# Optimization experiments

Hardware: AMD Instinct MI355X
Metric: run time of the kernel (lower is better)

Reference implementation:

```python
import jax, jax.numpy as jnp
import numpy as np

MIN_DEPTH, MAX_DEPTH = 0.1, 100.0
BN_EPS = 1e-5


def _conv(x, w, b, pad):
    y = jax.lax.conv_general_dilated(
        x, w, window_strides=(1, 1), padding=[(pad, pad), (pad, pad)],
        dimension_numbers=("NCHW", "OIHW", "NCHW"))
    return y + b[None, :, None, None]


def _bn(x, gamma, beta, mean, var):
    # eval-mode BatchNorm2d with running stats
    inv = jax.lax.rsqrt(var + BN_EPS)
    return (x - mean[None, :, None, None]) * (gamma * inv)[None, :, None, None] + beta[None, :, None, None]


def _object_depths(depth, bboxes):
    # depth: (B,1,H,W), bboxes: (B,N,4) int — per-box median (lower median, like torch)
    B, _, H, W = depth.shape
    xs = jnp.arange(W)
    ys = jnp.arange(H)

    def per_image(d2, boxes):  # d2: (H,W), boxes: (N,4)
        dflat = d2.reshape(-1)

        def one_box(box):
            x1 = jnp.maximum(box[0], 0)
            y1 = jnp.maximum(box[1], 0)
            x2 = jnp.minimum(box[2], W)
            y2 = jnp.minimum(box[3], H)
            mask = (((ys >= y1) & (ys < y2))[:, None] & ((xs >= x1) & (xs < x2))[None, :]).reshape(-1)
            vals = jnp.where(mask, dflat, jnp.inf)
            s = jnp.sort(vals)
            k = mask.sum()
            idx = jnp.maximum((k - 1) // 2, 0)
            med = jnp.take(s, idx)
            return jnp.where(k > 0, med, jnp.zeros((), dtype=d2.dtype))

        return jax.vmap(one_box)(boxes)

    return jax.vmap(per_image)(depth[:, 0], bboxes)


def _forward(features, bboxes, w1, b1, g1, be1, m1, v1, w2, b2, g2, be2, m2, v2,
             w3, b3, uw1, ub1, uw2, ub2):
    # depth head
    h = jax.nn.relu(_bn(_conv(features, w1, b1, 1), g1, be1, m1, v1))
    h = jax.nn.relu(_bn(_conv(h, w2, b2, 1), g2, be2, m2, v2))
    disp = jax.nn.sigmoid(_conv(h, w3, b3, 0))  # (B,1,H,W)
    min_disp = 1.0 / MAX_DEPTH
    max_disp = 1.0 / MIN_DEPTH
    depth = 1.0 / (min_disp + (max_disp - min_disp) * disp)
    # uncertainty head
    u = jax.nn.relu(_conv(features, uw1, ub1, 1))
    uncertainty = jax.nn.softplus(_conv(u, uw2, ub2, 0))
    obj = _object_depths(depth, bboxes)
    return depth, uncertainty, obj


def setup_inputs() -> dict:
    key = jax.random.key(0)
    ks = jax.random.split(key, 16)
    B, C, Hc, H, W, N = 8, 256, 256, 96, 160, 64
    f32 = jnp.float32
    inp = {
        "features": jax.random.normal(ks[0], (B, C, H, W), dtype=f32),
        "bboxes": jax.random.randint(ks[1], (B, N, 4), 0, 96, dtype=jnp.int32),
        "w1": jax.random.normal(ks[2], (Hc, C, 3, 3), dtype=f32) * 0.02,
        "b1": jnp.zeros((Hc,), f32),
        "g1": jnp.ones((Hc,), f32),
        "be1": jnp.zeros((Hc,), f32),
        "m1": jax.random.normal(ks[3], (Hc,), dtype=f32) * 0.1,
        "v1": jnp.ones((Hc,), f32),
        "w2": jax.random.normal(ks[4], (Hc, Hc, 3, 3), dtype=f32) * 0.02,
        "b2": jnp.zeros((Hc,), f32),
        "g2": jnp.ones((Hc,), f32),
        "be2": jnp.zeros((Hc,), f32),
        "m2": jax.random.normal(ks[5], (Hc,), dtype=f32) * 0.1,
        "v2": jnp.ones((Hc,), f32),
        "w3": jax.random.normal(ks[6], (1, Hc, 1, 1), dtype=f32) * 0.05,
        "b3": jnp.zeros((1,), f32),
        "uw1": jax.random.normal(ks[7], (Hc // 2, C, 3, 3), dtype=f32) * 0.02,
        "ub1": jnp.zeros((Hc // 2,), f32),
        "uw2": jax.random.normal(ks[8], (1, Hc // 2, 1, 1), dtype=f32) * 0.05,
        "ub2": jnp.zeros((1,), f32),
    }
    return inp


def reference(features, bboxes, w1, b1, g1, be1, m1, v1, w2, b2, g2, be2, m2, v2,
              w3, b3, uw1, ub1, uw2, ub2):
    return _forward(features, bboxes, w1, b1, g1, be1, m1, v1, w2, b2, g2, be2,
                    m2, v2, w3, b3, uw1, ub1, uw2, ub2)
```

## Files before the change

### kernel.cpp

```cpp
#include <hip/hip_runtime.h>
#include <hip/hip_bf16.h>

#define HH 96
#define WW 160
#define BATCH 8
#define NPIX (BATCH*HH*WW)
#define CIN 256
#define IMG (HH*WW)
#define PW 162
#define PH 98
#define PR (PH*PW)
#define PTOT (BATCH*PR)

typedef short bf16x8 __attribute__((ext_vector_type(8)));
typedef float f32x4 __attribute__((ext_vector_type(4)));

__device__ __forceinline__ unsigned short f2bf(float f) {
    unsigned int u = __float_as_uint(f);
    u = (u + 0x7fffu + ((u >> 16) & 1u)) >> 16;
    return (unsigned short)u;
}

__device__ __forceinline__ void gload16(const void* g, void* l) {
    __builtin_amdgcn_global_load_lds(
        (const __attribute__((address_space(1))) void*)g,
        (__attribute__((address_space(3))) void*)l,
        16, 0, 0);
}

__global__ __launch_bounds__(256) void prep_scalars(
    const float* __restrict__ b1, const float* __restrict__ g1, const float* __restrict__ be1,
    const float* __restrict__ m1, const float* __restrict__ v1,
    const float* __restrict__ b2, const float* __restrict__ g2, const float* __restrict__ be2,
    const float* __restrict__ m2, const float* __restrict__ v2,
    const float* __restrict__ ub1,
    float* __restrict__ scale1, float* __restrict__ bias1,
    float* __restrict__ scale2, float* __restrict__ bias2)
{
    int t = threadIdx.x;
    float s1 = g1[t] * rsqrtf(v1[t] + 1e-5f);
    scale1[t] = s1;
    bias1[t]  = (b1[t] - m1[t]) * s1 + be1[t];
    float s2 = g2[t] * rsqrtf(v2[t] + 1e-5f);
    scale2[t] = s2;
    bias2[t]  = (b2[t] - m2[t]) * s2 + be2[t];
    if (t < 128) { scale1[256 + t] = 1.0f; bias1[256 + t] = ub1[t]; }
}

__global__ __launch_bounds__(256) void prep_weights(
    const float* __restrict__ w1, const float* __restrict__ w2, const float* __restrict__ uw1,
    unsigned short* __restrict__ w1T, unsigned short* __restrict__ w2T, unsigned short* __restrict__ uw1T)
{
    const int S = 256 * 2304;
    int i = blockIdx.x * 256 + threadIdx.x;
    if (i < S) {
        int co = i / 2304, r = i % 2304, pos = r >> 8, ci = r & 255;
        w1T[i] = f2bf(w1[(co * 256 + ci) * 9 + pos]);
    } else if (i < 2 * S) {
        int j = i - S;
        int co = j / 2304, r = j % 2304, pos = r >> 8, ci = r & 255;
        w2T[j] = f2bf(w2[(co * 256 + ci) * 9 + pos]);
    } else {
        int j = i - 2 * S;
        int co = j / 2304, r = j % 2304, pos = r >> 8, ci = r & 255;
        uw1T[j] = f2bf(uw1[(co * 256 + ci) * 9 + pos]);
    }
}

__global__ __launch_bounds__(128) void zero_pads(
    unsigned int* __restrict__ featP, unsigned int* __restrict__ h1P)
{
    int bid = blockIdx.x;
    unsigned int* buf = (bid < 4128) ? featP : h1P;
    int k = (bid < 4128) ? bid : (bid - 4128);
    int img = k / 516, i = k % 516;
    int py, px;
    if (i < PW)            { py = 0;      px = i; }
    else if (i < 2 * PW)   { py = PH - 1; px = i - PW; }
    else { int q = i - 2 * PW; py = 1 + (q >> 1); px = (q & 1) ? (PW - 1) : 0; }
    size_t row = (size_t)img * PR + (size_t)py * PW + px;
    buf[row * 128 + threadIdx.x] = 0;
}

__global__ __launch_bounds__(256) void pack_features(
    const float* __restrict__ f, unsigned short* __restrict__ ft)
{
    __shared__ float tile[32][33];
    int x0 = blockIdx.x * 32;
    int c0 = blockIdx.y * 32;
    int by = blockIdx.z;
    int b = by / HH, y = by % HH;
    int tx = threadIdx.x & 31, tg = threadIdx.x >> 5;
    const float* src = f + (((size_t)(b * CIN + c0) * HH + y) * WW) + x0;
    #pragma unroll
    for (int i = 0; i < 4; ++i) {
        int cl = tg + i * 8;
        tile[cl][tx] = src[(size_t)cl * HH * WW + tx];
    }
    __syncthreads();
    size_t rbase = (size_t)b * PR + (size_t)(y + 1) * PW + (x0 + 1);
    #pragma unroll
    for (int i = 0; i < 4; ++i) {
        int xl = tg + i * 8;
        ft[(rbase + xl) * 256 + c0 + tx] = f2bf(tile[tx][xl]);
    }
}

__global__ __launch_bounds__(256, 3) void conv3x3_mfma(
    const unsigned short* __restrict__ inP,
    const unsigned short* __restrict__ wT,
    const float* __restrict__ scale, const float* __restrict__ bias,
    unsigned short* __restrict__ outT,
    float* __restrict__ uout,
    const float* __restrict__ uw2, const float* __restrict__ ub2,
    int Cout, int mode, int My)
{
    __shared__ unsigned short Alds[3 * 128 * 32];
    __shared__ unsigned short Blds[144 * 32];
    __shared__ float usum[2][128];

    const int t = threadIdx.x;
    const int wave = t >> 6;
    const int l = t & 63;

    const int lid = blockIdx.x;
    const int xcd = lid & 7;
    const int j = lid >> 3;
    const int n0 = (xcd * 120 + j / My) * 128;
    const int m0 = (j % My) * 128;
    const bool is_unc = (mode == 1) && (m0 == 256);

    const int b0 = n0 / IMG;
    const int rem0 = n0 % IMG;
    const int y0 = rem0 / WW;
    const int x0 = rem0 % WW;
    const int r0 = b0 * PR + (y0 + 1) * PW + (x0 + 1);

    const int lrow = l >> 2;
    const int lkq = (l & 3) ^ ((l >> 3) & 3);

    const unsigned short* asrc0 = wT + (size_t)(m0 + wave * 32 + lrow) * 9 * 256 + lkq * 8;
    const unsigned short* asrc1 = asrc0 + (size_t)16 * 9 * 256;

    char* AldsB = (char*)Alds;
    char* BldsB = (char*)Blds;
    char* aldst = AldsB + wave * 2048;

    const int wm = wave >> 1, wn = wave & 1;
    const int quad = l >> 4, lane16 = l & 15;
    const int aoff = lane16 * 64 + ((quad ^ ((lane16 >> 1) & 3)) << 4);

    int browbase[4];
    #pragma unroll
    for (int i = 0; i < 4; ++i) {
        int jj = wn * 64 + i * 16 + lane16;
        browbase[i] = jj + ((x0 + jj) >= WW ? 2 : 0) + 7;
    }

    f32x4 acc[4][4];
    #pragma unroll
    for (int mt = 0; mt < 4; ++mt)
        #pragma unroll
        for (int nt = 0; nt < 4; ++nt)
            acc[mt][nt] = (f32x4){0.f, 0.f, 0.f, 0.f};

    for (int cc = 0; cc < 8; ++cc) {
        const int ccoff = cc * 32;
        for (int dyi = 0; dyi < 3; ++dyi) {
            __syncthreads();
            const unsigned short* a0 = asrc0 + (dyi * 3) * 256 + ccoff;
            const unsigned short* a1 = asrc1 + (dyi * 3) * 256 + ccoff;
            #pragma unroll
            for (int dxp = 0; dxp < 3; ++dxp) {
                gload16(a0 + dxp * 256, aldst + dxp * 8192);
                gload16(a1 + dxp * 256, aldst + dxp * 8192 + 1024);
            }
            const ptrdiff_t rs = (ptrdiff_t)r0 + (ptrdiff_t)(dyi - 1) * PW - 8;
            const unsigned short* bs = inP + (rs + lrow) * 256 + ccoff + lkq * 8
                                           + (size_t)wave * 8192;
            gload16(bs, BldsB + wave * 2048);
            gload16(bs + 4096, BldsB + wave * 2048 + 1024);
            if (wave == 3) gload16(bs + 8192, BldsB + 8192);
            __syncthreads();
            #pragma unroll
            for (int dx = 0; dx < 3; ++dx) {
                bf16x8 af[4], bfr[4];
                #pragma unroll
                for (int mt = 0; mt < 4; ++mt)
                    af[mt] = *(const bf16x8*)(AldsB + dx * 8192 + ((wm * 4 + mt) << 10) + aoff);
                #pragma unroll
                for (int i = 0; i < 4; ++i) {
                    int row = browbase[i] + dx;
                    int ba = (row << 6) + ((quad ^ ((row >> 1) & 3)) << 4);
                    bfr[i] = *(const bf16x8*)(BldsB + ba);
                }
                #pragma unroll
                for (int mt = 0; mt < 4; ++mt)
                    #pragma unroll
                    for (int nt = 0; nt < 4; ++nt)
                        acc[mt][nt] = __builtin_amdgcn_mfma_f32_16x16x32_bf16(
                            af[mt], bfr[nt], acc[mt][nt], 0, 0, 0);
            }
        }
    }

    if (is_unc) {
        const float* ub = bias + 256;
        float s[4] = {0.f, 0.f, 0.f, 0.f};
        #pragma unroll
        for (int mt = 0; mt < 4; ++mt) {
            const int mg = wm * 64 + mt * 16 + quad * 4;
            const float4 bi = *(const float4*)&ub[mg];
            const float4 uw = *(const float4*)&uw2[mg];
            #pragma unroll
            for (int nt = 0; nt < 4; ++nt) {
                s[nt] += fmaxf(acc[mt][nt][0] + bi.x, 0.f) * uw.x
                       + fmaxf(acc[mt][nt][1] + bi.y, 0.f) * uw.y
                       + fmaxf(acc[mt][nt][2] + bi.z, 0.f) * uw.z
                       + fmaxf(acc[mt][nt][3] + bi.w, 0.f) * uw.w;
            }
        }
        #pragma unroll
        for (int nt = 0; nt < 4; ++nt) {
            s[nt] += __shfl_xor(s[nt], 16);
            s[nt] += __shfl_xor(s[nt], 32);
        }
        if (quad == 0) {
            #pragma unroll
            for (int nt = 0; nt < 4; ++nt)
                usum[wm][wn * 64 + nt * 16 + lane16] = s[nt];
        }
        __syncthreads();
        if (t < 128) {
            float x = usum[0][t] + usum[1][t] + ub2[0];
            uout[n0 + t] = fmaxf(x, 0.f) + log1pf(expf(-fabsf(x)));
        }
        return;
    }

    size_t obase[4];
    #pragma unroll
    for (int nt = 0; nt < 4; ++nt) {
        int n = n0 + wn * 64 + nt * 16 + lane16;
        if (mode == 1) {
            int b = n / IMG, rem = n % IMG, yy = rem / WW, xx = rem % WW;
            obase[nt] = ((size_t)(b * PH + yy + 1) * PW + (xx + 1)) * 256;
        } else {
            obase[nt] = (size_t)n * Cout;
        }
    }
    #pragma unroll
    for (int mt = 0; mt < 4; ++mt) {
        const int mg = m0 + wm * 64 + mt * 16 + quad * 4;
        const float4 sc = *(const float4*)&scale[mg];
        const float4 bi = *(const float4*)&bias[mg];
        #pragma unroll
        for (int nt = 0; nt < 4; ++nt) {
            ushort4 pk;
            pk.x = f2bf(fmaxf(acc[mt][nt][0] * sc.x + bi.x, 0.f));
            pk.y = f2bf(fmaxf(acc[mt][nt][1] * sc.y + bi.y, 0.f));
            pk.z = f2bf(fmaxf(acc[mt][nt][2] * sc.z + bi.z, 0.f));
            pk.w = f2bf(fmaxf(acc[mt][nt][3] * sc.w + bi.w, 0.f));
            *(ushort4*)&outT[obase[nt] + mg] = pk;
        }
    }
}

__global__ __launch_bounds__(256) void head_depth(
    const unsigned short* __restrict__ h2, const float* __restrict__ w3,
    const float* __restrict__ b3, float* __restrict__ out)
{
    __shared__ float ws[256];
    ws[threadIdx.x] = w3[threadIdx.x];
    __syncthreads();
    const int pix = blockIdx.x * 64 + (threadIdx.x >> 2);
    const int q = threadIdx.x & 3;
    const unsigned short* p = h2 + (size_t)pix * 256 + q * 64;
    float s = 0.f;
    #pragma unroll
    for (int i = 0; i < 64; i += 8) {
        uint4 v = *(const uint4*)(p + i);
        const float* wq = &ws[q * 64 + i];
        s += __uint_as_float(v.x << 16) * wq[0];
        s += __uint_as_float(v.x & 0xffff0000u) * wq[1];
        s += __uint_as_float(v.y << 16) * wq[2];
        s += __uint_as_float(v.y & 0xffff0000u) * wq[3];
        s += __uint_as_float(v.z << 16) * wq[4];
        s += __uint_as_float(v.z & 0xffff0000u) * wq[5];
        s += __uint_as_float(v.w << 16) * wq[6];
        s += __uint_as_float(v.w & 0xffff0000u) * wq[7];
    }
    s += __shfl_xor(s, 1);
    s += __shfl_xor(s, 2);
    if (q == 0) {
        float x = s + b3[0];
        float sig = 1.f / (1.f + expf(-x));
        out[pix] = 1.f / (0.01f + 9.99f * sig);
    }
}

__global__ __launch_bounds__(256) void median_kernel(
    const float* __restrict__ depth, const int* __restrict__ bboxes, float* __restrict__ obj)
{
    const int bi = blockIdx.x;
    const int b = bi >> 6;
    const int* bb = bboxes + (size_t)bi * 4;
    int x1 = max(bb[0], 0), y1 = max(bb[1], 0);
    int x2 = min(bb[2], WW), y2 = min(bb[3], HH);
    int w = x2 - x1, h = y2 - y1;
    if (w <= 0 || h <= 0) {
        if (threadIdx.x == 0) obj[bi] = 0.f;
        return;
    }
    const int wh = w * h;
    int tgt = (wh - 1) >> 1;
    const float* dbase = depth + (size_t)b * HH * WW;

    __shared__ unsigned int hist[256];
    __shared__ unsigned int sel_prefix, sel_target;
    unsigned int prefix = 0;

    for (int pass = 0; pass < 4; ++pass) {
        const int shift = 24 - 8 * pass;
        hist[threadIdx.x] = 0;
        __syncthreads();
        const unsigned int mask_high = (pass == 0) ? 0u : (0xFFFFFFFFu << (shift + 8));
        for (int idx = threadIdx.x; idx < wh; idx += 256) {
            int yy = y1 + idx / w, xx = x1 + idx % w;
            unsigned int uu = __float_as_uint(dbase[yy * WW + xx]);
            if ((uu & mask_high) == (prefix & mask_high))
                atomicAdd(&hist[(uu >> shift) & 255], 1u);
        }
        __syncthreads();
        if (threadIdx.x == 0) {
            unsigned int cum = 0;
            for (int bin = 0; bin < 256; ++bin) {
                unsigned int c = hist[bin];
                if (cum + c > (unsigned int)tgt) {
                    sel_target = (unsigned int)tgt - cum;
                    sel_prefix = prefix | ((unsigned int)bin << shift);
                    break;
                }
                cum += c;
            }
        }
        __syncthreads();
        prefix = sel_prefix;
        tgt = (int)sel_target;
    }
    if (threadIdx.x == 0) obj[bi] = __uint_as_float(prefix);
}

extern "C" void kernel_launch(void* const* d_in, const int* in_sizes, int n_in,
                              void* d_out, int out_size, void* d_ws, size_t ws_size,
                              hipStream_t stream) {
    const float* features = (const float*)d_in[0];
    const int*   bboxes   = (const int*)d_in[1];
    const float* w1  = (const float*)d_in[2];
    const float* b1  = (const float*)d_in[3];
    const float* g1  = (const float*)d_in[4];
    const float* be1 = (const float*)d_in[5];
    const float* m1  = (const float*)d_in[6];
    const float* v1  = (const float*)d_in[7];
    const float* w2  = (const float*)d_in[8];
    const float* b2  = (const float*)d_in[9];
    const float* g2  = (const float*)d_in[10];
    const float* be2 = (const float*)d_in[11];
    const float* m2  = (const float*)d_in[12];
    const float* v2  = (const float*)d_in[13];
    const float* w3  = (const float*)d_in[14];
    const float* b3  = (const float*)d_in[15];
    const float* uw1 = (const float*)d_in[16];
    const float* ub1 = (const float*)d_in[17];
    const float* uw2 = (const float*)d_in[18];
    const float* ub2 = (const float*)d_in[19];
    float* out = (float*)d_out;

    char* ws = (char*)d_ws;
    unsigned short* featP = (unsigned short*)(ws + 8192);
    unsigned short* h1P   = (unsigned short*)(ws + 65044480);
    unsigned short* h2    = (unsigned short*)(ws + 8192);
    unsigned short* w1T   = (unsigned short*)(ws + 130080768);
    unsigned short* uw1T  = w1T + 256 * 2304;
    unsigned short* w2T   = uw1T + 128 * 2304;
    float* scale1 = (float*)(w2T + 589824);
    float* bias1  = scale1 + 384;
    float* scale2 = bias1 + 384;
    float* bias2  = scale2 + 256;

    prep_scalars<<<1, 256, 0, stream>>>(b1, g1, be1, m1, v1, b2, g2, be2, m2, v2, ub1,
                                        scale1, bias1, scale2, bias2);
    prep_weights<<<5760, 256, 0, stream>>>(w1, w2, uw1, w1T, w2T, uw1T);
    zero_pads<<<8256, 128, 0, stream>>>((unsigned int*)featP, (unsigned int*)h1P);
    pack_features<<<dim3(WW / 32, CIN / 32, BATCH * HH), 256, 0, stream>>>(features, featP);

    conv3x3_mfma<<<2880, 256, 0, stream>>>(
        featP, w1T, scale1, bias1, h1P, out + NPIX, uw2, ub2, 256, 1, 3);
    conv3x3_mfma<<<1920, 256, 0, stream>>>(
        h1P, w2T, scale2, bias2, h2, nullptr, nullptr, nullptr, 256, 0, 2);

    head_depth<<<NPIX / 64, 256, 0, stream>>>(h2, w3, b3, out);
    median_kernel<<<BATCH * 64, 256, 0, stream>>>(out, bboxes, out + 2 * NPIX);
}
```

Measured before the change: 649.7 us.

## Fuse depth 1x1 projection into conv2 epilogue with atomic reduction

The second conv now computes the 1x1 depth projection directly in its epilogue: each block reduces BN+ReLU outputs against w3 and atomically adds its partial dot product into a zero-initialized depth buffer, so the bf16 h2 tensor is never written or reread. A small elementwise kernel then applies the bias, sigmoid and depth mapping. The zero_pads kernel additionally clears the depth output. The first conv also gets a higher min-waves launch bound (4 instead of 3), which may force register spilling. Atomics make the summation order nondeterministic.

Measured after the change: 629.1 us. 1.03x faster.

```diff
diff --git a/kernel.cpp b/kernel.cpp
--- a/kernel.cpp
+++ b/kernel.cpp
@@ -68,18 +68,23 @@
 }
 
 __global__ __launch_bounds__(128) void zero_pads(
-    unsigned int* __restrict__ featP, unsigned int* __restrict__ h1P)
+    unsigned int* __restrict__ featP, unsigned int* __restrict__ h1P, float* __restrict__ outd)
 {
     int bid = blockIdx.x;
-    unsigned int* buf = (bid < 4128) ? featP : h1P;
-    int k = (bid < 4128) ? bid : (bid - 4128);
-    int img = k / 516, i = k % 516;
-    int py, px;
-    if (i < PW)            { py = 0;      px = i; }
-    else if (i < 2 * PW)   { py = PH - 1; px = i - PW; }
-    else { int q = i - 2 * PW; py = 1 + (q >> 1); px = (q & 1) ? (PW - 1) : 0; }
-    size_t row = (size_t)img * PR + (size_t)py * PW + px;
-    buf[row * 128 + threadIdx.x] = 0;
+    if (bid < 8256) {
+        unsigned int* buf = (bid < 4128) ? featP : h1P;
+        int k = (bid < 4128) ? bid : (bid - 4128);
+        int img = k / 516, i = k % 516;
+        int py, px;
+        if (i < PW)            { py = 0;      px = i; }
+        else if (i < 2 * PW)   { py = PH - 1; px = i - PW; }
+        else { int q = i - 2 * PW; py = 1 + (q >> 1); px = (q & 1) ? (PW - 1) : 0; }
+        size_t row = (size_t)img * PR + (size_t)py * PW + px;
+        buf[row * 128 + threadIdx.x] = 0;
+    } else {
+        int k = bid - 8256;
+        outd[(size_t)k * 128 + threadIdx.x] = 0.f;
+    }
 }
 
 __global__ __launch_bounds__(256) void pack_features(
@@ -106,7 +111,8 @@
     }
 }
 
-__global__ __launch_bounds__(256, 3) void conv3x3_mfma(
+template<int MINW>
+__global__ __launch_bounds__(256, MINW) void conv3x3_mfma(
     const unsigned short* __restrict__ inP,
     const unsigned short* __restrict__ wT,
     const float* __restrict__ scale, const float* __restrict__ bias,
@@ -238,16 +244,43 @@
         return;
     }
 
+    if (mode == 0) {
+        float s[4] = {0.f, 0.f, 0.f, 0.f};
+        #pragma unroll
+        for (int mt = 0; mt < 4; ++mt) {
+            const int mg = m0 + wm * 64 + mt * 16 + quad * 4;
+            const float4 sc = *(const float4*)&scale[mg];
+            const float4 bi = *(const float4*)&bias[mg];
+            const float4 w  = *(const float4*)&uw2[mg];
+            #pragma unroll
+            for (int nt = 0; nt < 4; ++nt) {
+                s[nt] += fmaxf(acc[mt][nt][0] * sc.x + bi.x, 0.f) * w.x
+                       + fmaxf(acc[mt][nt][1] * sc.y + bi.y, 0.f) * w.y
+                       + fmaxf(acc[mt][nt][2] * sc.z + bi.z, 0.f) * w.z
+                       + fmaxf(acc[mt][nt][3] * sc.w + bi.w, 0.f) * w.w;
+            }
+        }
+        #pragma unroll
+        for (int nt = 0; nt < 4; ++nt) {
+            s[nt] += __shfl_xor(s[nt], 16);
+            s[nt] += __shfl_xor(s[nt], 32);
+        }
+        if (quad == 0) {
+            #pragma unroll
+            for (int nt = 0; nt < 4; ++nt)
+                usum[wm][wn * 64 + nt * 16 + lane16] = s[nt];
+        }
+        __syncthreads();
+        if (t < 128) atomicAdd(&uout[n0 + t], usum[0][t] + usum[1][t]);
+        return;
+    }
+
     size_t obase[4];
     #pragma unroll
     for (int nt = 0; nt < 4; ++nt) {
         int n = n0 + wn * 64 + nt * 16 + lane16;
-        if (mode == 1) {
-            int b = n / IMG, rem = n % IMG, yy = rem / WW, xx = rem % WW;
-            obase[nt] = ((size_t)(b * PH + yy + 1) * PW + (xx + 1)) * 256;
-        } else {
-            obase[nt] = (size_t)n * Cout;
-        }
+        int b = n / IMG, rem = n % IMG, yy = rem / WW, xx = rem % WW;
+        obase[nt] = ((size_t)(b * PH + yy + 1) * PW + (xx + 1)) * 256;
     }
     #pragma unroll
     for (int mt = 0; mt < 4; ++mt) {
@@ -266,37 +299,13 @@
     }
 }
 
-__global__ __launch_bounds__(256) void head_depth(
-    const unsigned short* __restrict__ h2, const float* __restrict__ w3,
-    const float* __restrict__ b3, float* __restrict__ out)
-{
-    __shared__ float ws[256];
-    ws[threadIdx.x] = w3[threadIdx.x];
-    __syncthreads();
-    const int pix = blockIdx.x * 64 + (threadIdx.x >> 2);
-    const int q = threadIdx.x & 3;
-    const unsigned short* p = h2 + (size_t)pix * 256 + q * 64;
-    float s = 0.f;
-    #pragma unroll
-    for (int i = 0; i < 64; i += 8) {
-        uint4 v = *(const uint4*)(p + i);
-        const float* wq = &ws[q * 64 + i];
-        s += __uint_as_float(v.x << 16) * wq[0];
-        s += __uint_as_float(v.x & 0xffff0000u) * wq[1];
-        s += __uint_as_float(v.y << 16) * wq[2];
-        s += __uint_as_float(v.y & 0xffff0000u) * wq[3];
-        s += __uint_as_float(v.z << 16) * wq[4];
-        s += __uint_as_float(v.z & 0xffff0000u) * wq[5];
-        s += __uint_as_float(v.w << 16) * wq[6];
-        s += __uint_as_float(v.w & 0xffff0000u) * wq[7];
-    }
-    s += __shfl_xor(s, 1);
-    s += __shfl_xor(s, 2);
-    if (q == 0) {
-        float x = s + b3[0];
-        float sig = 1.f / (1.f + expf(-x));
-        out[pix] = 1.f / (0.01f + 9.99f * sig);
-    }
+__global__ __launch_bounds__(256) void depth_transform(
+    float* __restrict__ out, const float* __restrict__ b3)
+{
+    int i = blockIdx.x * 256 + threadIdx.x;
+    float x = out[i] + b3[0];
+    float sig = 1.f / (1.f + expf(-x));
+    out[i] = 1.f / (0.01f + 9.99f * sig);
 }
 
 __global__ __launch_bounds__(256) void median_kernel(
@@ -379,7 +388,6 @@
     char* ws = (char*)d_ws;
     unsigned short* featP = (unsigned short*)(ws + 8192);
     unsigned short* h1P   = (unsigned short*)(ws + 65044480);
-    unsigned short* h2    = (unsigned short*)(ws + 8192);
     unsigned short* w1T   = (unsigned short*)(ws + 130080768);
     unsigned short* uw1T  = w1T + 256 * 2304;
     unsigned short* w2T   = uw1T + 128 * 2304;
@@ -391,14 +399,14 @@
     prep_scalars<<<1, 256, 0, stream>>>(b1, g1, be1, m1, v1, b2, g2, be2, m2, v2, ub1,
                                         scale1, bias1, scale2, bias2);
     prep_weights<<<5760, 256, 0, stream>>>(w1, w2, uw1, w1T, w2T, uw1T);
-    zero_pads<<<8256, 128, 0, stream>>>((unsigned int*)featP, (unsigned int*)h1P);
+    zero_pads<<<9216, 128, 0, stream>>>((unsigned int*)featP, (unsigned int*)h1P, out);
     pack_features<<<dim3(WW / 32, CIN / 32, BATCH * HH), 256, 0, stream>>>(features, featP);
 
-    conv3x3_mfma<<<2880, 256, 0, stream>>>(
+    conv3x3_mfma<4><<<2880, 256, 0, stream>>>(
         featP, w1T, scale1, bias1, h1P, out + NPIX, uw2, ub2, 256, 1, 3);
-    conv3x3_mfma<<<1920, 256, 0, stream>>>(
-        h1P, w2T, scale2, bias2, h2, nullptr, nullptr, nullptr, 256, 0, 2);
-
-    head_depth<<<NPIX / 64, 256, 0, stream>>>(h2, w3, b3, out);
+    conv3x3_mfma<3><<<1920, 256, 0, stream>>>(
+        h1P, w2T, scale2, bias2, nullptr, out, w3, nullptr, 256, 0, 2);
+
+    depth_transform<<<NPIX / 256, 256, 0, stream>>>(out, b3);
     median_kernel<<<BATCH * 64, 256, 0, stream>>>(out, bboxes, out + 2 * NPIX);
 }
```
